# Performance work log

Hardware: AMD Instinct MI355X
Metric: run time of the kernel (lower is better)

Reference implementation:

```python
import jax, jax.numpy as jnp
import numpy as np

B, N, T, H = 64, 15, 256, 128
TEMP = 1.0


def setup_inputs() -> dict:
    key = jax.random.key(0)
    ks = jax.random.split(key, 5)
    node_output = jax.random.normal(ks[0], (B, T, H), jnp.float32)
    neigh_output = jax.random.normal(ks[1], (B, N, T, H), jnp.float32)
    # causal-style mask: True = masked (t' > t); guarantees no fully-masked row
    attn_mask = jnp.broadcast_to(jnp.triu(jnp.ones((T, T), bool), k=1), (B, T, T))
    xav = (2.0 / (H + H)) ** 0.5  # xavier_normal std for square HxH
    Wq = jax.random.normal(ks[2], (H, H), jnp.float32) * xav
    Wk = jax.random.normal(ks[3], (H, H), jnp.float32) * xav
    Wv = jax.random.normal(ks[4], (H, H), jnp.float32) * xav
    z = jnp.zeros((H,), jnp.float32)  # biases init to 0 in init_params
    return dict(node_output=node_output, neigh_output=neigh_output,
                neighbors_number=N, attn_mask=attn_mask,
                Wq=Wq, bq=z, Wk=Wk, bk=z, Wv=Wv, bv=z)


def reference(node_output, neigh_output, neighbors_number, attn_mask,
              Wq, bq, Wk, bk, Wv, bv):
    b, t, h = node_output.shape
    n = neigh_output.shape[1]
    # key/value sequence: self node followed by its n neighbors -> [B, N+1, T, H]
    kv = jnp.concatenate([node_output[:, None], neigh_output], axis=1)
    # Linear (torch convention y = x W^T + b); query repeat collapses to single proj
    q = node_output @ Wq.T + bq                      # [B, T, H]
    k = kv @ Wk.T + bk                               # [B, N+1, T, H]
    v = kv.reshape(b, (n + 1) * t, h) @ Wv.T + bv    # [B, (N+1)*T, H]
    # scores: each query attends separately to every (source, timestep) key
    S = jnp.einsum('bth,bnsh->bnts', q, k)           # [B, N+1, T, T]
    # S_norm computed on the PRE-mask scores (original norms S.data before fill)
    S_norm = jnp.linalg.norm(S.reshape(b, -1), axis=-1)  # [B]
    S = jnp.where(attn_mask[:, None, :, :], -jnp.inf, S)
    S = jnp.transpose(S, (0, 2, 1, 3)) / TEMP        # [B, T, N+1, T]
    # joint softmax over all (N+1)*T keys at once
    A = jax.nn.softmax(S.reshape(b, t, (n + 1) * t), axis=-1)
    out = jnp.einsum('btk,bkh->bth', A, v)           # [B, T, H]
    return out, A.reshape(b, t, n + 1, t), S_norm
```

## Files before the change

kernel.cpp:

```cpp
#include <hip/hip_runtime.h>
#include <math.h>


constexpr int BB   = 64;
constexpr int TT   = 256;
constexpr int HH   = 128;
constexpr int KEYS = 4096;
constexpr int LDK  = 136;
constexpr int LDV  = 72;
constexpr float SOFF = 20.f;

typedef __attribute__((ext_vector_type(8)))  __bf16 bf16x8;
typedef __attribute__((ext_vector_type(16))) float  f32x16;
typedef __attribute__((ext_vector_type(4)))  float  f32x4;
typedef __attribute__((ext_vector_type(4)))  unsigned u32x4;
typedef unsigned short ushort_t;

__device__ __forceinline__ float4 ld4(const float* p) {
  return *reinterpret_cast<const float4*>(p);
}
__device__ __forceinline__ ushort_t f2bf(float x) {
  union { __bf16 b; ushort_t u; } c; c.b = (__bf16)x; return c.u;
}
__device__ __forceinline__ float bf2f(ushort_t h) {
  return __uint_as_float(((unsigned)h) << 16);
}
__device__ __forceinline__ void splitf(float x, ushort_t& h, ushort_t& l) {
  h = f2bf(x);
  l = f2bf(x - bf2f(h));
}
__device__ __forceinline__ f32x16 zero16() {
  f32x16 z;
  #pragma unroll
  for (int i = 0; i < 16; ++i) z[i] = 0.f;
  return z;
}
__device__ __forceinline__ f32x16 mfma3(bf16x8 ahi, bf16x8 alo,
                                        bf16x8 bhi, bf16x8 blo, f32x16 c) {
  c = __builtin_amdgcn_mfma_f32_32x32x16_bf16(ahi, bhi, c, 0, 0, 0);
  c = __builtin_amdgcn_mfma_f32_32x32x16_bf16(ahi, blo, c, 0, 0, 0);
  c = __builtin_amdgcn_mfma_f32_32x32x16_bf16(alo, bhi, c, 0, 0, 0);
  return c;
}

__global__ __launch_bounds__(256) void prep_w_kernel(
    const float* __restrict__ Wq, const float* __restrict__ Wk,
    const float* __restrict__ Wv,
    ushort_t* __restrict__ wqh, ushort_t* __restrict__ wql,
    ushort_t* __restrict__ wkh, ushort_t* __restrict__ wkl,
    ushort_t* __restrict__ wvh, ushort_t* __restrict__ wvl)
{
  int i = blockIdx.x * 256 + threadIdx.x;
  if (i >= HH * HH) return;
  ushort_t h, l;
  splitf(Wq[i], h, l); wqh[i] = h; wql[i] = l;
  splitf(Wk[i], h, l); wkh[i] = h; wkl[i] = l;
  splitf(Wv[i], h, l); wvh[i] = h; wvl[i] = l;
}

template<bool DOV>
__global__ __launch_bounds__(256, 4) void proj_kernel(
    const float* __restrict__ node, const float* __restrict__ neigh,
    const ushort_t* __restrict__ W1h, const ushort_t* __restrict__ W1l,
    const float* __restrict__ b1,
    const ushort_t* __restrict__ WVh, const ushort_t* __restrict__ WVl,
    const float* __restrict__ bV,
    ushort_t* __restrict__ yh, ushort_t* __restrict__ yl,
    ushort_t* __restrict__ v_t, int mode)
{
  __shared__ ushort_t xh[64 * LDK];
  __shared__ ushort_t xl[64 * LDK];
  const int tid = threadIdx.x;
  const long r0 = (long)blockIdx.x * 64;

  #pragma unroll
  for (int i = 0; i < 8; ++i) {
    int slot = tid + 256 * i;
    int row = slot >> 5, h0 = (slot & 31) << 2;
    long r = r0 + row;
    const float* src;
    if (mode == 0) {
      src = node + r * HH;
    } else {
      long bb = r >> 12;
      int  n  = (int)((r >> 8) & 15);
      int  t  = (int)(r & 255);
      src = (n == 0) ? (node + (bb * TT + t) * HH)
                     : (neigh + ((bb * 15 + (n - 1)) * (long)TT + t) * HH);
    }
    float4 xv = ld4(src + h0);
    ushort_t h0h, h0l, h1h, h1l, h2h, h2l, h3h, h3l;
    splitf(xv.x, h0h, h0l); splitf(xv.y, h1h, h1l);
    splitf(xv.z, h2h, h2l); splitf(xv.w, h3h, h3l);
    *reinterpret_cast<uint2*>(&xh[row * LDK + h0]) =
        make_uint2((unsigned)h0h | ((unsigned)h1h << 16),
                   (unsigned)h2h | ((unsigned)h3h << 16));
    *reinterpret_cast<uint2*>(&xl[row * LDK + h0]) =
        make_uint2((unsigned)h0l | ((unsigned)h1l << 16),
                   (unsigned)h2l | ((unsigned)h3l << 16));
  }
  __syncthreads();

  const int l = tid & 63, w = tid >> 6, g = l >> 5, lane31 = l & 31;
  const int j = 32 * w + lane31;

  f32x16 accK[2];
  #pragma unroll
  for (int kt = 0; kt < 2; ++kt) accK[kt] = zero16();
  f32x16 accV[2];
  if constexpr (DOV) {
    #pragma unroll
    for (int kt = 0; kt < 2; ++kt) accV[kt] = zero16();
  }

  #pragma unroll
  for (int hs = 0; hs < 8; ++hs) {
    const int ho = 16 * hs + 8 * g;
    bf16x8 wh = *reinterpret_cast<const bf16x8*>(W1h + j * HH + ho);
    bf16x8 wl = *reinterpret_cast<const bf16x8*>(W1l + j * HH + ho);
    bf16x8 xhf[2], xlf[2];
    #pragma unroll
    for (int rt = 0; rt < 2; ++rt) {
      xhf[rt] = *reinterpret_cast<const bf16x8*>(&xh[(32 * rt + lane31) * LDK + ho]);
      xlf[rt] = *reinterpret_cast<const bf16x8*>(&xl[(32 * rt + lane31) * LDK + ho]);
    }
    #pragma unroll
    for (int rt = 0; rt < 2; ++rt)
      accK[rt] = mfma3(xhf[rt], xlf[rt], wh, wl, accK[rt]);
    if constexpr (DOV) {
      bf16x8 vh = *reinterpret_cast<const bf16x8*>(WVh + j * HH + ho);
      #pragma unroll
      for (int rt = 0; rt < 2; ++rt) {
        accV[rt] = __builtin_amdgcn_mfma_f32_32x32x16_bf16(vh, xhf[rt], accV[rt], 0, 0, 0);
        accV[rt] = __builtin_amdgcn_mfma_f32_32x32x16_bf16(vh, xlf[rt], accV[rt], 0, 0, 0);
      }
    }
  }

  const float bK = b1[j];
  #pragma unroll
  for (int kt = 0; kt < 2; ++kt) {
    #pragma unroll
    for (int reg = 0; reg < 16; ++reg) {
      int rm = (reg & 3) + 8 * (reg >> 2) + 4 * g;
      long r = r0 + 32 * kt + rm;
      ushort_t h, lo_;
      splitf(accK[kt][reg] + bK, h, lo_);
      yh[r * HH + j] = h;
      yl[r * HH + j] = lo_;
    }
  }
  if constexpr (DOV) {
    const int bidx = (int)(r0 >> 12);
    const int key0 = (int)(r0 & (KEYS - 1));
    float bvr[16];
    #pragma unroll
    for (int reg = 0; reg < 16; ++reg)
      bvr[reg] = bV[32 * w + (reg & 3) + 8 * (reg >> 2) + 4 * g];
    #pragma unroll
    for (int kt = 0; kt < 2; ++kt) {
      #pragma unroll
      for (int reg = 0; reg < 16; ++reg) {
        int rm = (reg & 3) + 8 * (reg >> 2) + 4 * g;
        int jrow = 32 * w + rm;
        v_t[((long)(bidx * HH + jrow)) * KEYS + key0 + 32 * kt + lane31] =
            f2bf(accV[kt][reg] + bvr[reg]);
      }
    }
  }
}

__global__ __launch_bounds__(256, 2) void passX_kernel(
    const ushort_t* __restrict__ q_hi, const ushort_t* __restrict__ q_lo,
    const ushort_t* __restrict__ k_hi, const ushort_t* __restrict__ k_lo,
    const ushort_t* __restrict__ v_t,
    ushort_t* __restrict__ P_out, float* __restrict__ l_part,
    float* __restrict__ ssq_part, float* __restrict__ opart)
{
  __shared__ ushort_t Khi[64 * LDK];
  __shared__ ushort_t Klo[64 * LDK];
  __shared__ ushort_t Vt[128 * LDV];
  __shared__ ushort_t As[64 * LDV];
  __shared__ float redS[4];
  const int tid = threadIdx.x, l = tid & 63, w = tid >> 6;
  const int g = (l >> 5) & 1, lane31 = l & 31;
  const int wt = w & 1, wk = w >> 1;
  const int p = blockIdx.x;
  const int xcd = p & 7, slot = p >> 3;
  const int pair = xcd * 16 + (slot >> 2);
  const int tq = slot & 3;
  const int b = pair >> 1, ksb = pair & 1;
  const int t0 = tq * 64;

  bf16x8 qhi[8], qlo[8];
  {
    const long qb = ((long)(b * TT + t0 + 32 * wt + lane31)) * HH;
    #pragma unroll
    for (int hs = 0; hs < 8; ++hs) {
      qhi[hs] = *reinterpret_cast<const bf16x8*>(q_hi + qb + 16 * hs + 8 * g);
      qlo[hs] = *reinterpret_cast<const bf16x8*>(q_lo + qb + 16 * hs + 8 * g);
    }
  }

  float lreg[16];
  #pragma unroll
  for (int r = 0; r < 16; ++r) lreg[r] = 0.f;
  float ssq = 0.f;
  f32x16 o0 = zero16(), o1 = zero16();

  for (int kt = 0; kt < 32; ++kt) {
    const int kb = ksb * 2048 + kt * 64;
    const bool live = (kb & 255) <= (t0 | 63);

    __syncthreads();
    #pragma unroll
    for (int i = 0; i < 4; ++i) {
      int s2 = i * 256 + tid;
      int row = s2 >> 4, c0 = (s2 & 15) << 3;
      const long gsrc = ((long)(b * KEYS + kb + row)) * HH + c0;
      *reinterpret_cast<uint4*>(&Khi[row * LDK + c0]) =
          *reinterpret_cast<const uint4*>(k_hi + gsrc);
      *reinterpret_cast<uint4*>(&Klo[row * LDK + c0]) =
          *reinterpret_cast<const uint4*>(k_lo + gsrc);
    }
    if (live) {
      #pragma unroll
      for (int i = 0; i < 4; ++i) {
        int s2 = i * 256 + tid;
        int hh = s2 >> 3, k0 = (s2 & 7) << 3;
        *reinterpret_cast<uint4*>(&Vt[hh * LDV + k0]) =
            *reinterpret_cast<const uint4*>(
                v_t + ((long)(b * HH + hh)) * KEYS + kb + k0);
      }
    }
    __syncthreads();

    __builtin_amdgcn_s_setprio(1);
    f32x16 accA = zero16(), accB = zero16();
    #pragma unroll
    for (int hp = 0; hp < 4; ++hp) {
      const int hoA = 16 * (2 * hp) + 8 * g;
      const int hoB = 16 * (2 * hp + 1) + 8 * g;
      bf16x8 khA = *reinterpret_cast<const bf16x8*>(
          &Khi[(32 * wk + lane31) * LDK + hoA]);
      bf16x8 klA = *reinterpret_cast<const bf16x8*>(
          &Klo[(32 * wk + lane31) * LDK + hoA]);
      bf16x8 khB = *reinterpret_cast<const bf16x8*>(
          &Khi[(32 * wk + lane31) * LDK + hoB]);
      bf16x8 klB = *reinterpret_cast<const bf16x8*>(
          &Klo[(32 * wk + lane31) * LDK + hoB]);
      accA = mfma3(qhi[2 * hp],     qlo[2 * hp],     khA, klA, accA);
      accB = mfma3(qhi[2 * hp + 1], qlo[2 * hp + 1], khB, klB, accB);
    }
    __builtin_amdgcn_s_setprio(0);

    if (live) {
      const int key = kb + 32 * wk + lane31;
      const int st = key & 255;
      #pragma unroll
      for (int reg = 0; reg < 16; ++reg) {
        const int rl = 32 * wt + (reg & 3) + 8 * (reg >> 2) + 4 * g;
        const int tr = t0 + rl;
        float s = accA[reg] + accB[reg];
        ssq = fmaf(s, s, ssq);
        float pv_ = (st <= tr) ? __expf(s - SOFF) : 0.f;
        lreg[reg] += pv_;
        As[rl * LDV + 32 * wk + lane31] = f2bf(pv_);
      }
      __syncthreads();

      #pragma unroll
      for (int c = 0; c < 2; ++c) {
        int s3 = c * 256 + tid;
        int row = s3 >> 3, col = (s3 & 7) << 3;
        *reinterpret_cast<uint4*>(
            P_out + ((long)(b * TT + t0 + row)) * KEYS + kb + col) =
            *reinterpret_cast<const uint4*>(&As[row * LDV + col]);
      }

      __builtin_amdgcn_s_setprio(1);
      #pragma unroll
      for (int ksx = 0; ksx < 4; ++ksx) {
        const int ko = 16 * ksx + 8 * g;
        bf16x8 af = *reinterpret_cast<const bf16x8*>(
            &As[(32 * wt + lane31) * LDV + ko]);
        bf16x8 v0 = *reinterpret_cast<const bf16x8*>(
            &Vt[(64 * wk + lane31) * LDV + ko]);
        bf16x8 v1 = *reinterpret_cast<const bf16x8*>(
            &Vt[(64 * wk + 32 + lane31) * LDV + ko]);
        o0 = __builtin_amdgcn_mfma_f32_32x32x16_bf16(af, v0, o0, 0, 0, 0);
        o1 = __builtin_amdgcn_mfma_f32_32x32x16_bf16(af, v1, o1, 0, 0, 0);
      }
      __builtin_amdgcn_s_setprio(0);
    } else {
      #pragma unroll
      for (int reg = 0; reg < 16; ++reg) {
        float s = accA[reg] + accB[reg];
        ssq = fmaf(s, s, ssq);
      }
    }
  }

  #pragma unroll
  for (int reg = 0; reg < 16; ++reg) {
    #pragma unroll
    for (int off = 1; off < 32; off <<= 1)
      lreg[reg] += __shfl_xor(lreg[reg], off);
  }
  if (lane31 == 0) {
    const int slotL = ksb * 2 + wk;
    #pragma unroll
    for (int reg = 0; reg < 16; ++reg) {
      const int tr = t0 + 32 * wt + (reg & 3) + 8 * (reg >> 2) + 4 * g;
      l_part[slotL * (BB * TT) + b * TT + tr] = lreg[reg];
    }
  }

  #pragma unroll
  for (int off = 1; off < 64; off <<= 1) ssq += __shfl_xor(ssq, off);
  if (l == 0) redS[w] = ssq;
  __syncthreads();
  if (tid == 0)
    ssq_part[b * 8 + tq * 2 + ksb] = redS[0] + redS[1] + redS[2] + redS[3];

  #pragma unroll
  for (int reg = 0; reg < 16; ++reg) {
    const int tr = t0 + 32 * wt + (reg & 3) + 8 * (reg >> 2) + 4 * g;
    long base = (long)ksb * (BB * TT * HH) + ((long)(b * TT + tr)) * HH + 64 * wk;
    opart[base + lane31]      = o0[reg];
    opart[base + 32 + lane31] = o1[reg];
  }
}

__global__ __launch_bounds__(256) void passY_kernel(
    const ushort_t* __restrict__ P_in, const float* __restrict__ l_part,
    float* __restrict__ A_out)
{
  const long total = (long)BB * TT * KEYS / 8;
  for (long u = (long)blockIdx.x * 256 + threadIdx.x; u < total;
       u += (long)gridDim.x * 256) {
    const int row = (int)(u >> 9);
    const int t = row & 255;
    const int s0 = ((int)(u & 511) << 3) & 255;
    f32x4 a0, a1;
    if (s0 > t) {
      a0 = (f32x4){0.f, 0.f, 0.f, 0.f};
      a1 = a0;
    } else {
      const float L = l_part[row] + l_part[BB * TT + row] +
                      l_part[2 * BB * TT + row] + l_part[3 * BB * TT + row];
      const float s = 1.0f / L;
      u32x4 pv = __builtin_nontemporal_load(
          reinterpret_cast<const u32x4*>(P_in + u * 8));
      a0.x = bf2f((ushort_t)(pv.x & 0xffff)) * s;
      a0.y = bf2f((ushort_t)(pv.x >> 16)) * s;
      a0.z = bf2f((ushort_t)(pv.y & 0xffff)) * s;
      a0.w = bf2f((ushort_t)(pv.y >> 16)) * s;
      a1.x = bf2f((ushort_t)(pv.z & 0xffff)) * s;
      a1.y = bf2f((ushort_t)(pv.z >> 16)) * s;
      a1.z = bf2f((ushort_t)(pv.w & 0xffff)) * s;
      a1.w = bf2f((ushort_t)(pv.w >> 16)) * s;
    }
    __builtin_nontemporal_store(a0, reinterpret_cast<f32x4*>(A_out + u * 8));
    __builtin_nontemporal_store(a1, reinterpret_cast<f32x4*>(A_out + u * 8 + 4));
  }
}

__global__ void reduce_out_kernel(const float* __restrict__ opart,
                                  const float* __restrict__ l_part,
                                  float* __restrict__ out)
{
  int i = blockIdx.x * 256 + threadIdx.x;
  const int n4 = BB * TT * HH / 4;
  if (i >= n4) return;
  const int row = i >> 5;
  const float L = l_part[row] + l_part[BB * TT + row] +
                  l_part[2 * BB * TT + row] + l_part[3 * BB * TT + row];
  const float s = 1.0f / L;
  const float4* p0 = reinterpret_cast<const float4*>(opart);
  const float4* p1 = reinterpret_cast<const float4*>(opart + (long)BB * TT * HH);
  float4 a = p0[i], c = p1[i];
  a.x = (a.x + c.x) * s;
  a.y = (a.y + c.y) * s;
  a.z = (a.z + c.z) * s;
  a.w = (a.w + c.w) * s;
  *reinterpret_cast<float4*>(out + 4 * (long)i) = a;
}

__global__ void finalize_kernel(const float* __restrict__ ssq_part,
                                float* __restrict__ S_norm)
{
  int b = threadIdx.x;
  if (b < BB) {
    float s = 0.f;
    #pragma unroll
    for (int i = 0; i < 8; ++i) s += ssq_part[b * 8 + i];
    S_norm[b] = sqrtf(s);
  }
}

extern "C" void kernel_launch(void* const* d_in, const int* in_sizes, int n_in,
                              void* d_out, int out_size, void* d_ws, size_t ws_size,
                              hipStream_t stream)
{
  const float* node  = (const float*)d_in[0];
  const float* neigh = (const float*)d_in[1];
  const float* Wq = (const float*)d_in[4];
  const float* bq = (const float*)d_in[5];
  const float* Wk = (const float*)d_in[6];
  const float* bk = (const float*)d_in[7];
  const float* Wv = (const float*)d_in[8];
  const float* bv = (const float*)d_in[9];

  float* out    = (float*)d_out;
  float* A_out  = out + (long)BB * TT * HH;
  float* S_norm = A_out + (long)BB * TT * KEYS;

  ushort_t* q_hi = (ushort_t*)d_ws;
  ushort_t* q_lo = q_hi + (long)BB * TT * HH;
  ushort_t* k_hi = q_lo + (long)BB * TT * HH;
  ushort_t* k_lo = k_hi + (long)BB * KEYS * HH;
  ushort_t* v_t  = k_lo + (long)BB * KEYS * HH;
  ushort_t* wqh  = v_t + (long)BB * HH * KEYS;
  ushort_t* wql  = wqh + HH * HH;
  ushort_t* wkh  = wql + HH * HH;
  ushort_t* wkl  = wkh + HH * HH;
  ushort_t* wvh  = wkl + HH * HH;
  ushort_t* wvl  = wvh + HH * HH;
  ushort_t* P_ws = wvl + HH * HH;
  float* l_part  = (float*)(P_ws + (long)BB * TT * KEYS);
  float* ssq_part = l_part + 4 * BB * TT;
  float* opart   = ssq_part + 512;

  prep_w_kernel<<<dim3((HH * HH + 255) / 256), dim3(256), 0, stream>>>(
      Wq, Wk, Wv, wqh, wql, wkh, wkl, wvh, wvl);
  proj_kernel<false><<<dim3(BB * TT / 64), dim3(256), 0, stream>>>(
      node, neigh, wqh, wql, bq, wvh, wvl, bv, q_hi, q_lo, v_t, 0);
  proj_kernel<true><<<dim3(BB * KEYS / 64), dim3(256), 0, stream>>>(
      node, neigh, wkh, wkl, bk, wvh, wvl, bv, k_hi, k_lo, v_t, 1);
  passX_kernel<<<dim3(BB * 8), dim3(256), 0, stream>>>(
      q_hi, q_lo, k_hi, k_lo, v_t, P_ws, l_part, ssq_part, opart);
  passY_kernel<<<dim3(4096), dim3(256), 0, stream>>>(P_ws, l_part, A_out);
  reduce_out_kernel<<<dim3((BB * TT * HH / 4 + 255) / 256), dim3(256), 0, stream>>>(
      opart, l_part, out);
  finalize_kernel<<<dim3(1), dim3(64), 0, stream>>>(ssq_part, S_norm);
}
```

Measured before the change: 340.8 us.

## Skip masked key tiles and compute score norm via Gram matrices

The Frobenius norm of the pre-mask scores is computed in a separate kernel as the inner product of the K and Q Gram matrices, so the attention pass no longer has to score masked tiles. The attention pass now launches only blocks covering causally live key-position groups, with per-query-tile work split into variable numbers of partial slots. The reductions for l and the output sum the variable number of partials. The norm uses only bf16 high parts, which reduces precision, and adds a kernel launch.

```diff
diff --git a/kernel.cpp b/kernel.cpp
--- a/kernel.cpp
+++ b/kernel.cpp
@@ -8,6 +8,7 @@
 constexpr int KEYS = 4096;
 constexpr int LDK  = 136;
 constexpr int LDV  = 72;
+constexpr int LDG  = 136;
 constexpr float SOFF = 20.f;
 
 typedef __attribute__((ext_vector_type(8)))  __bf16 bf16x8;
@@ -170,26 +171,114 @@
   }
 }
 
+__global__ __launch_bounds__(256) void gram_kernel(
+    const ushort_t* __restrict__ q_hi, const ushort_t* __restrict__ k_hi,
+    float* __restrict__ ssq_part)
+{
+  __shared__ ushort_t tr[128 * LDG];
+  __shared__ float red[4];
+  const int tid = threadIdx.x, l = tid & 63, w = tid >> 6;
+  const int g = (l >> 5) & 1, lane31 = l & 31;
+  const int p = blockIdx.x;
+  const int gidx = (p & 7) * 32 + (p >> 3);
+  const int b = gidx >> 2, piece = gidx & 3;
+
+  f32x16 acck[4], accq[4];
+  #pragma unroll
+  for (int j = 0; j < 4; ++j) { acck[j] = zero16(); accq[j] = zero16(); }
+
+  for (int c = 0; c < 8; ++c) {
+    const long sbase = (long)b * KEYS + piece * 1024 + c * 128;
+    __syncthreads();
+    #pragma unroll
+    for (int i = 0; i < 8; ++i) {
+      int slot = i * 256 + tid;
+      int srow = slot >> 4, h0 = (slot & 15) << 3;
+      uint4 v = *reinterpret_cast<const uint4*>(k_hi + (sbase + srow) * HH + h0);
+      const unsigned* pv = reinterpret_cast<const unsigned*>(&v);
+      #pragma unroll
+      for (int e2 = 0; e2 < 4; ++e2) {
+        unsigned u = pv[e2];
+        tr[(h0 + 2 * e2    ) * LDG + srow] = (ushort_t)(u & 0xffff);
+        tr[(h0 + 2 * e2 + 1) * LDG + srow] = (ushort_t)(u >> 16);
+      }
+    }
+    __syncthreads();
+    #pragma unroll
+    for (int ss = 0; ss < 8; ++ss) {
+      const int so = ss * 16 + 8 * g;
+      bf16x8 A = *reinterpret_cast<const bf16x8*>(&tr[(32 * w + lane31) * LDG + so]);
+      #pragma unroll
+      for (int j = 0; j < 4; ++j) {
+        bf16x8 Bf = *reinterpret_cast<const bf16x8*>(&tr[(32 * j + lane31) * LDG + so]);
+        acck[j] = __builtin_amdgcn_mfma_f32_32x32x16_bf16(A, Bf, acck[j], 0, 0, 0);
+      }
+    }
+  }
+  for (int c = 0; c < 2; ++c) {
+    const long sbase = (long)b * TT + c * 128;
+    __syncthreads();
+    #pragma unroll
+    for (int i = 0; i < 8; ++i) {
+      int slot = i * 256 + tid;
+      int srow = slot >> 4, h0 = (slot & 15) << 3;
+      uint4 v = *reinterpret_cast<const uint4*>(q_hi + (sbase + srow) * HH + h0);
+      const unsigned* pv = reinterpret_cast<const unsigned*>(&v);
+      #pragma unroll
+      for (int e2 = 0; e2 < 4; ++e2) {
+        unsigned u = pv[e2];
+        tr[(h0 + 2 * e2    ) * LDG + srow] = (ushort_t)(u & 0xffff);
+        tr[(h0 + 2 * e2 + 1) * LDG + srow] = (ushort_t)(u >> 16);
+      }
+    }
+    __syncthreads();
+    #pragma unroll
+    for (int ss = 0; ss < 8; ++ss) {
+      const int so = ss * 16 + 8 * g;
+      bf16x8 A = *reinterpret_cast<const bf16x8*>(&tr[(32 * w + lane31) * LDG + so]);
+      #pragma unroll
+      for (int j = 0; j < 4; ++j) {
+        bf16x8 Bf = *reinterpret_cast<const bf16x8*>(&tr[(32 * j + lane31) * LDG + so]);
+        accq[j] = __builtin_amdgcn_mfma_f32_32x32x16_bf16(A, Bf, accq[j], 0, 0, 0);
+      }
+    }
+  }
+
+  float dot = 0.f;
+  #pragma unroll
+  for (int j = 0; j < 4; ++j)
+    #pragma unroll
+    for (int reg = 0; reg < 16; ++reg)
+      dot = fmaf(acck[j][reg], accq[j][reg], dot);
+  #pragma unroll
+  for (int off = 1; off < 64; off <<= 1) dot += __shfl_xor(dot, off);
+  if (l == 0) red[w] = dot;
+  __syncthreads();
+  if (tid == 0) ssq_part[b * 4 + piece] = red[0] + red[1] + red[2] + red[3];
+}
+
 __global__ __launch_bounds__(256, 2) void passX_kernel(
     const ushort_t* __restrict__ q_hi, const ushort_t* __restrict__ q_lo,
     const ushort_t* __restrict__ k_hi, const ushort_t* __restrict__ k_lo,
     const ushort_t* __restrict__ v_t,
     ushort_t* __restrict__ P_out, float* __restrict__ l_part,
-    float* __restrict__ ssq_part, float* __restrict__ opart)
+    float* __restrict__ opart)
 {
   __shared__ ushort_t Khi[64 * LDK];
   __shared__ ushort_t Klo[64 * LDK];
   __shared__ ushort_t Vt[128 * LDV];
   __shared__ ushort_t As[64 * LDV];
-  __shared__ float redS[4];
   const int tid = threadIdx.x, l = tid & 63, w = tid >> 6;
   const int g = (l >> 5) & 1, lane31 = l & 31;
   const int wt = w & 1, wk = w >> 1;
   const int p = blockIdx.x;
-  const int xcd = p & 7, slot = p >> 3;
-  const int pair = xcd * 16 + (slot >> 2);
-  const int tq = slot & 3;
-  const int b = pair >> 1, ksb = pair & 1;
+  const int gidx = (p & 7) * 80 + (p >> 3);
+  const int b = gidx / 10, off = gidx % 10;
+  int tq, q;
+  if (off < 1)      { tq = 0; q = 0; }
+  else if (off < 3) { tq = 1; q = off - 1; }
+  else if (off < 6) { tq = 2; q = off - 3; }
+  else              { tq = 3; q = off - 6; }
   const int t0 = tq * 64;
 
   bf16x8 qhi[8], qlo[8];
@@ -205,13 +294,10 @@
   float lreg[16];
   #pragma unroll
   for (int r = 0; r < 16; ++r) lreg[r] = 0.f;
-  float ssq = 0.f;
   f32x16 o0 = zero16(), o1 = zero16();
 
-  for (int kt = 0; kt < 32; ++kt) {
-    const int kb = ksb * 2048 + kt * 64;
-    const bool live = (kb & 255) <= (t0 | 63);
-
+  for (int kt8 = 0; kt8 < 16; ++kt8) {
+    const int kb = (kt8 * 4 + q) * 64;
     __syncthreads();
     #pragma unroll
     for (int i = 0; i < 4; ++i) {
@@ -223,15 +309,13 @@
       *reinterpret_cast<uint4*>(&Klo[row * LDK + c0]) =
           *reinterpret_cast<const uint4*>(k_lo + gsrc);
     }
-    if (live) {
-      #pragma unroll
-      for (int i = 0; i < 4; ++i) {
-        int s2 = i * 256 + tid;
-        int hh = s2 >> 3, k0 = (s2 & 7) << 3;
-        *reinterpret_cast<uint4*>(&Vt[hh * LDV + k0]) =
-            *reinterpret_cast<const uint4*>(
-                v_t + ((long)(b * HH + hh)) * KEYS + kb + k0);
-      }
+    #pragma unroll
+    for (int i = 0; i < 4; ++i) {
+      int s2 = i * 256 + tid;
+      int hh = s2 >> 3, k0 = (s2 & 7) << 3;
+      *reinterpret_cast<uint4*>(&Vt[hh * LDV + k0]) =
+          *reinterpret_cast<const uint4*>(
+              v_t + ((long)(b * HH + hh)) * KEYS + kb + k0);
     }
     __syncthreads();
 
@@ -254,61 +338,52 @@
     }
     __builtin_amdgcn_s_setprio(0);
 
-    if (live) {
-      const int key = kb + 32 * wk + lane31;
-      const int st = key & 255;
-      #pragma unroll
-      for (int reg = 0; reg < 16; ++reg) {
-        const int rl = 32 * wt + (reg & 3) + 8 * (reg >> 2) + 4 * g;
-        const int tr = t0 + rl;
-        float s = accA[reg] + accB[reg];
-        ssq = fmaf(s, s, ssq);
-        float pv_ = (st <= tr) ? __expf(s - SOFF) : 0.f;
-        lreg[reg] += pv_;
-        As[rl * LDV + 32 * wk + lane31] = f2bf(pv_);
-      }
-      __syncthreads();
-
-      #pragma unroll
-      for (int c = 0; c < 2; ++c) {
-        int s3 = c * 256 + tid;
-        int row = s3 >> 3, col = (s3 & 7) << 3;
-        *reinterpret_cast<uint4*>(
-            P_out + ((long)(b * TT + t0 + row)) * KEYS + kb + col) =
-            *reinterpret_cast<const uint4*>(&As[row * LDV + col]);
-      }
-
-      __builtin_amdgcn_s_setprio(1);
-      #pragma unroll
-      for (int ksx = 0; ksx < 4; ++ksx) {
-        const int ko = 16 * ksx + 8 * g;
-        bf16x8 af = *reinterpret_cast<const bf16x8*>(
-            &As[(32 * wt + lane31) * LDV + ko]);
-        bf16x8 v0 = *reinterpret_cast<const bf16x8*>(
-            &Vt[(64 * wk + lane31) * LDV + ko]);
-        bf16x8 v1 = *reinterpret_cast<const bf16x8*>(
-            &Vt[(64 * wk + 32 + lane31) * LDV + ko]);
-        o0 = __builtin_amdgcn_mfma_f32_32x32x16_bf16(af, v0, o0, 0, 0, 0);
-        o1 = __builtin_amdgcn_mfma_f32_32x32x16_bf16(af, v1, o1, 0, 0, 0);
-      }
-      __builtin_amdgcn_s_setprio(0);
-    } else {
-      #pragma unroll
-      for (int reg = 0; reg < 16; ++reg) {
-        float s = accA[reg] + accB[reg];
-        ssq = fmaf(s, s, ssq);
-      }
-    }
+    const int key = kb + 32 * wk + lane31;
+    const int st = key & 255;
+    #pragma unroll
+    for (int reg = 0; reg < 16; ++reg) {
+      const int rl = 32 * wt + (reg & 3) + 8 * (reg >> 2) + 4 * g;
+      const int tr = t0 + rl;
+      float s = accA[reg] + accB[reg];
+      float pv_ = (st <= tr) ? __expf(s - SOFF) : 0.f;
+      lreg[reg] += pv_;
+      As[rl * LDV + 32 * wk + lane31] = f2bf(pv_);
+    }
+    __syncthreads();
+
+    #pragma unroll
+    for (int c = 0; c < 2; ++c) {
+      int s3 = c * 256 + tid;
+      int row = s3 >> 3, col = (s3 & 7) << 3;
+      *reinterpret_cast<uint4*>(
+          P_out + ((long)(b * TT + t0 + row)) * KEYS + kb + col) =
+          *reinterpret_cast<const uint4*>(&As[row * LDV + col]);
+    }
+
+    __builtin_amdgcn_s_setprio(1);
+    #pragma unroll
+    for (int ksx = 0; ksx < 4; ++ksx) {
+      const int ko = 16 * ksx + 8 * g;
+      bf16x8 af = *reinterpret_cast<const bf16x8*>(
+          &As[(32 * wt + lane31) * LDV + ko]);
+      bf16x8 v0 = *reinterpret_cast<const bf16x8*>(
+          &Vt[(64 * wk + lane31) * LDV + ko]);
+      bf16x8 v1 = *reinterpret_cast<const bf16x8*>(
+          &Vt[(64 * wk + 32 + lane31) * LDV + ko]);
+      o0 = __builtin_amdgcn_mfma_f32_32x32x16_bf16(af, v0, o0, 0, 0, 0);
+      o1 = __builtin_amdgcn_mfma_f32_32x32x16_bf16(af, v1, o1, 0, 0, 0);
+    }
+    __builtin_amdgcn_s_setprio(0);
   }
 
   #pragma unroll
   for (int reg = 0; reg < 16; ++reg) {
     #pragma unroll
-    for (int off = 1; off < 32; off <<= 1)
-      lreg[reg] += __shfl_xor(lreg[reg], off);
+    for (int offx = 1; offx < 32; offx <<= 1)
+      lreg[reg] += __shfl_xor(lreg[reg], offx);
   }
   if (lane31 == 0) {
-    const int slotL = ksb * 2 + wk;
+    const int slotL = q * 2 + wk;
     #pragma unroll
     for (int reg = 0; reg < 16; ++reg) {
       const int tr = t0 + 32 * wt + (reg & 3) + 8 * (reg >> 2) + 4 * g;
@@ -317,16 +392,9 @@
   }
 
   #pragma unroll
-  for (int off = 1; off < 64; off <<= 1) ssq += __shfl_xor(ssq, off);
-  if (l == 0) redS[w] = ssq;
-  __syncthreads();
-  if (tid == 0)
-    ssq_part[b * 8 + tq * 2 + ksb] = redS[0] + redS[1] + redS[2] + redS[3];
-
-  #pragma unroll
   for (int reg = 0; reg < 16; ++reg) {
     const int tr = t0 + 32 * wt + (reg & 3) + 8 * (reg >> 2) + 4 * g;
-    long base = (long)ksb * (BB * TT * HH) + ((long)(b * TT + tr)) * HH + 64 * wk;
+    long base = (long)q * (BB * TT * HH) + ((long)(b * TT + tr)) * HH + 64 * wk;
     opart[base + lane31]      = o0[reg];
     opart[base + 32 + lane31] = o1[reg];
   }
@@ -347,8 +415,9 @@
       a0 = (f32x4){0.f, 0.f, 0.f, 0.f};
       a1 = a0;
     } else {
-      const float L = l_part[row] + l_part[BB * TT + row] +
-                      l_part[2 * BB * TT + row] + l_part[3 * BB * TT + row];
+      const int nslot = 2 * (t >> 6) + 2;
+      float L = 0.f;
+      for (int qq = 0; qq < nslot; ++qq) L += l_part[qq * (BB * TT) + row];
       const float s = 1.0f / L;
       u32x4 pv = __builtin_nontemporal_load(
           reinterpret_cast<const u32x4*>(P_in + u * 8));
@@ -374,16 +443,18 @@
   const int n4 = BB * TT * HH / 4;
   if (i >= n4) return;
   const int row = i >> 5;
-  const float L = l_part[row] + l_part[BB * TT + row] +
-                  l_part[2 * BB * TT + row] + l_part[3 * BB * TT + row];
+  const int t = row & 255;
+  const int nq = t >> 6;
+  float L = 0.f;
+  for (int qq = 0; qq < 2 * nq + 2; ++qq) L += l_part[qq * (BB * TT) + row];
   const float s = 1.0f / L;
-  const float4* p0 = reinterpret_cast<const float4*>(opart);
-  const float4* p1 = reinterpret_cast<const float4*>(opart + (long)BB * TT * HH);
-  float4 a = p0[i], c = p1[i];
-  a.x = (a.x + c.x) * s;
-  a.y = (a.y + c.y) * s;
-  a.z = (a.z + c.z) * s;
-  a.w = (a.w + c.w) * s;
+  float4 a = make_float4(0.f, 0.f, 0.f, 0.f);
+  for (int qq = 0; qq <= nq; ++qq) {
+    const float4 c = reinterpret_cast<const float4*>(
+        opart + (long)qq * (BB * TT * HH))[i];
+    a.x += c.x; a.y += c.y; a.z += c.z; a.w += c.w;
+  }
+  a.x *= s; a.y *= s; a.z *= s; a.w *= s;
   *reinterpret_cast<float4*>(out + 4 * (long)i) = a;
 }
 
@@ -392,9 +463,8 @@
 {
   int b = threadIdx.x;
   if (b < BB) {
-    float s = 0.f;
-    #pragma unroll
-    for (int i = 0; i < 8; ++i) s += ssq_part[b * 8 + i];
+    float s = ssq_part[b * 4] + ssq_part[b * 4 + 1] +
+              ssq_part[b * 4 + 2] + ssq_part[b * 4 + 3];
     S_norm[b] = sqrtf(s);
   }
 }
@@ -429,8 +499,8 @@
   ushort_t* wvl  = wvh + HH * HH;
   ushort_t* P_ws = wvl + HH * HH;
   float* l_part  = (float*)(P_ws + (long)BB * TT * KEYS);
-  float* ssq_part = l_part + 4 * BB * TT;
-  float* opart   = ssq_part + 512;
+  float* ssq_part = l_part + 8 * BB * TT;
+  float* opart   = ssq_part + 256;
 
   prep_w_kernel<<<dim3((HH * HH + 255) / 256), dim3(256), 0, stream>>>(
       Wq, Wk, Wv, wqh, wql, wkh, wkl, wvh, wvl);
@@ -438,8 +508,9 @@
       node, neigh, wqh, wql, bq, wvh, wvl, bv, q_hi, q_lo, v_t, 0);
   proj_kernel<true><<<dim3(BB * KEYS / 64), dim3(256), 0, stream>>>(
       node, neigh, wkh, wkl, bk, wvh, wvl, bv, k_hi, k_lo, v_t, 1);
-  passX_kernel<<<dim3(BB * 8), dim3(256), 0, stream>>>(
-      q_hi, q_lo, k_hi, k_lo, v_t, P_ws, l_part, ssq_part, opart);
+  gram_kernel<<<dim3(256), dim3(256), 0, stream>>>(q_hi, k_hi, ssq_part);
+  passX_kernel<<<dim3(640), dim3(256), 0, stream>>>(
+      q_hi, q_lo, k_hi, k_lo, v_t, P_ws, l_part, opart);
   passY_kernel<<<dim3(4096), dim3(256), 0, stream>>>(P_ws, l_part, A_out);
   reduce_out_kernel<<<dim3((BB * TT * HH / 4 + 255) / 256), dim3(256), 0, stream>>>(
       opart, l_part, out);
```

New measurement: 404.5 us. +18.7%, slower.
